# Performance work log

Hardware: AMD Instinct MI355X
Metric: run time of the kernel (lower is better)

Reference implementation:

```python
import jax, jax.numpy as jnp
import numpy as np

IN, OUT, STEPS, BATCH = 1024, 1024, 100, 64
THR = 15.0
RATIO = 0.5
C1 = RATIO * THR            # initial membrane potential = 7.5
C2 = 1.0 / THR
C3 = (1.0 - RATIO) / STEPS


def setup_inputs() -> dict:
    key = jax.random.key(0)
    k0, k1, k2, k3 = jax.random.split(key, 4)
    spikes = jax.random.randint(k0, (STEPS, BATCH, IN), 0, 2).astype(jnp.float32)
    mem = jnp.full((BATCH, OUT), C1, dtype=jnp.float32)          # init_if
    hat_spikes = jax.random.uniform(k1, (BATCH, IN), dtype=jnp.float32)
    W = jax.random.normal(k2, (OUT, IN), dtype=jnp.float32)      # w_mean=0, w_std=1
    b = jax.random.normal(k3, (OUT,), dtype=jnp.float32)
    return {"spikes": spikes, "mem": mem, "hat_spikes": hat_spikes, "W": W, "b": b}


def reference(spikes, mem, hat_spikes, W, b):
    steps = spikes.shape[0]
    # delta_us = fc(spikes): [T, B, OUT]
    delta_us = jnp.einsum('tbi,oi->tbo', spikes, W) + b

    def step(carry, du):
        m, su = carry
        m = m + du
        s = (m > THR).astype(m.dtype)          # spike
        m = jnp.clip(m, 0.0, THR)              # clamp_(0, thr)
        su = su + m                            # sum_u += mem
        m = m - m * s                          # reset fired neurons
        return (m, su), s

    (mem_out, sum_u), ss = jax.lax.scan(
        step, (mem, jnp.zeros_like(mem)), delta_us)

    hat_u_fwd = sum_u / steps                  # [B, OUT]
    hat_s_fwd = ss.mean(axis=0)                # [B, OUT]

    # training-mode surrogate path: forward values come from the spike loop,
    # gradients flow through fc(hat_spikes) (ForwardFirstBackwardSecond)
    delta_u = hat_spikes @ W.T + b
    hat_u = jax.lax.stop_gradient(hat_u_fwd) + delta_u - jax.lax.stop_gradient(delta_u)
    surr = jnp.maximum(hat_u * C2, C3)         # (hat_u*C2).clamp_min(C3)
    hat_s = jax.lax.stop_gradient(hat_s_fwd) + surr - jax.lax.stop_gradient(surr)

    return ss, mem_out, hat_s
```

## Files before the change

kernel.cpp:

```cpp
#include <hip/hip_runtime.h>


typedef __attribute__((ext_vector_type(4))) int int4v;

#define T_STEPS 100
#define BO 65536
#define K_DIM 1024
#define A8_OFF 0
#define BT_OFF 6553600
#define LO_OFF 11796480

__global__ __launch_bounds__(256)
void prepass(const float* __restrict__ S, const float* __restrict__ W,
             signed char* __restrict__ A8, signed char* __restrict__ Bt) {
    const int wave = blockIdx.x * 4 + (threadIdx.x >> 6);
    const int lane = threadIdx.x & 63;
    const int r16 = lane & 15, quad = lane >> 4;

    if (wave < 6400) {
        const int m16 = wave >> 4, k64 = wave & 15;
        const int m = m16 * 16 + r16;
        const float* sp = S + (size_t)m * K_DIM + k64 * 64 + quad * 16;
        const float4 s0 = *(const float4*)(sp);
        const float4 s1 = *(const float4*)(sp + 4);
        const float4 s2 = *(const float4*)(sp + 8);
        const float4 s3 = *(const float4*)(sp + 12);
        const float sv[16] = {s0.x,s0.y,s0.z,s0.w, s1.x,s1.y,s1.z,s1.w,
                              s2.x,s2.y,s2.z,s2.w, s3.x,s3.y,s3.z,s3.w};
        union { signed char c[16]; int4v v; } u;
#pragma unroll
        for (int e = 0; e < 16; ++e) u.c[e] = (signed char)sv[e];
        *(int4v*)(A8 + ((size_t)(m16 * 16 + k64) * 1024) + lane * 16) = u.v;
    } else {
        const int t2 = wave - 6400;
        const int n16 = t2 >> 4, k64 = t2 & 15;
        const int n = n16 * 16 + r16;
        const float* wp = W + (size_t)n * K_DIM + k64 * 64 + quad * 16;
        const float4 w0 = *(const float4*)(wp);
        const float4 w1 = *(const float4*)(wp + 4);
        const float4 w2 = *(const float4*)(wp + 8);
        const float4 w3 = *(const float4*)(wp + 12);
        const float wv[16] = {w0.x,w0.y,w0.z,w0.w, w1.x,w1.y,w1.z,w1.w,
                              w2.x,w2.y,w2.z,w2.w, w3.x,w3.y,w3.z,w3.w};
        union { signed char c[16]; int4v v; } u[4];
#pragma unroll
        for (int e = 0; e < 16; ++e) {
            long long q = llrint((double)wv[e] * 0x1p28);
#pragma unroll
            for (int p = 0; p < 3; ++p) {
                const int d = (int)(((q + 128) & 255) - 128);
                u[p].c[e] = (signed char)d;
                q = (q - d) >> 8;
            }
            u[3].c[e] = (signed char)q;
        }
        signed char* base = Bt + (size_t)(n16 * 16 + k64) * 4 * 1024 + lane * 16;
#pragma unroll
        for (int p = 0; p < 4; ++p)
            *(int4v*)(base + (size_t)p * 1024) = u[p].v;
    }
}

__global__ __launch_bounds__(256)
void gemm_i8(const signed char* __restrict__ A8,
             const signed char* __restrict__ Bt,
             const float* __restrict__ bias,
             float* __restrict__ Chi,
             _Float16* __restrict__ Lo) {
    const int bid = blockIdx.x;
    const int xcd = bid & 7;
    const int t_  = bid >> 3;
    const int cu  = t_ & 31;
    const int rnd = t_ >> 5;
    const int bn = (xcd << 2) | (cu & 3);
    const int bm = (cu >> 2) + (rnd << 3);

    const int tid = threadIdx.x;
    const int lane = tid & 63, wid = tid >> 6;
    const int wm = wid >> 1, wn = wid & 1;
    const int quad = lane >> 4, r16 = lane & 15;
    const int mgb = bm * 8 + wm * 4;
    const int ng  = bn * 2 + wn;

    const signed char* Ab = A8 + (size_t)mgb * 16384 + (size_t)lane * 16;
    const signed char* Bb = Bt + (size_t)ng * 65536 + (size_t)lane * 16;

    int4v av[3][4], bv[3][4];
    int4v acc[4][4] = {};

    auto loadS = [&](int kt, int s) {
#pragma unroll
        for (int i = 0; i < 4; ++i)
            av[s][i] = *(const int4v*)(Ab + (size_t)(i * 16 + kt) * 1024);
#pragma unroll
        for (int p = 0; p < 4; ++p)
            bv[s][p] = *(const int4v*)(Bb + (size_t)(kt * 4 + p) * 1024);
    };
    auto mf = [&](int s) {
#pragma unroll
        for (int p = 0; p < 4; ++p)
#pragma unroll
            for (int i = 0; i < 4; ++i)
                acc[i][p] = __builtin_amdgcn_mfma_i32_16x16x64_i8(
                    av[s][i], bv[s][p], acc[i][p], 0, 0, 0);
    };

    loadS(0, 0);
    loadS(1, 1);
#pragma unroll
    for (int kt = 0; kt < 16; ++kt) {
        if (kt + 2 < 16) loadS(kt + 2, (kt + 2) % 3);
        mf(kt % 3);
    }

    const int n_g = bn * 32 + wn * 16 + r16;
    const double bd = (double)bias[n_g];
#pragma unroll
    for (int i = 0; i < 4; ++i)
#pragma unroll
        for (int e = 0; e < 4; ++e) {
            long long t = (long long)acc[i][3][e];
            t = t * 256 + (long long)acc[i][2][e];
            t = t * 256 + (long long)acc[i][1][e];
            t = t * 256 + (long long)acc[i][0][e];
            const double du = (double)t * 0x1p-28 + bd;
            const float hi = (float)du;
            const float lo = (float)(du - (double)hi);
            const size_t m_g = (size_t)(bm * 128 + wm * 64 + i * 16 + quad * 4 + e);
            const size_t off = m_g * 1024 + n_g;
            Chi[off] = hi;
            Lo[off] = (_Float16)(lo * 4096.0f);
        }
}

__global__ __launch_bounds__(256)
void snn_scan(float* __restrict__ out, const _Float16* __restrict__ lo,
              const float* __restrict__ mem0) {
    const int bo = blockIdx.x * 256 + threadIdx.x;
    double m = (double)mem0[bo];
    double cnt = 0.0;
    float h[4][4], l[4][4];
#pragma unroll
    for (int s = 0; s < 3; ++s)
#pragma unroll
        for (int u = 0; u < 4; ++u) {
            const size_t idx = (size_t)(s * 4 + u) * BO + bo;
            h[s][u] = out[idx];
            l[s][u] = (float)lo[idx];
        }
#pragma unroll
    for (int g = 0; g < 25; ++g) {
        const int cs = g & 3, ps = (g + 3) & 3;
        if (g + 3 < 25) {
#pragma unroll
            for (int u = 0; u < 4; ++u) {
                const size_t idx = (size_t)((g + 3) * 4 + u) * BO + bo;
                h[ps][u] = out[idx];
                l[ps][u] = (float)lo[idx];
            }
        }
#pragma unroll
        for (int u = 0; u < 4; ++u) {
            const double du = (double)h[cs][u] + (double)l[cs][u] * 0x1p-12;
            m += du;
            const double s = (m > 15.0) ? 1.0 : 0.0;
            m = fmin(fmax(m, 0.0), 15.0);
            out[(size_t)(g * 4 + u) * BO + bo] = (float)s;
            cnt += s;
            m -= m * s;
        }
    }
    out[(size_t)T_STEPS * BO + bo] = (float)m;
    out[(size_t)(T_STEPS + 1) * BO + bo] = (float)(cnt * 0.01);
}

extern "C" void kernel_launch(void* const* d_in, const int* in_sizes, int n_in,
                              void* d_out, int out_size, void* d_ws, size_t ws_size,
                              hipStream_t stream) {
    const float* spikes = (const float*)d_in[0];
    const float* mem    = (const float*)d_in[1];
    const float* W      = (const float*)d_in[3];
    const float* b      = (const float*)d_in[4];
    float* out = (float*)d_out;
    signed char* A8 = (signed char*)d_ws + A8_OFF;
    signed char* Bt = (signed char*)d_ws + BT_OFF;
    _Float16*    Lo = (_Float16*)((char*)d_ws + LO_OFF);

    prepass<<<dim3(1856), 256, 0, stream>>>(spikes, W, A8, Bt);
    gemm_i8<<<dim3(1600), 256, 0, stream>>>(A8, Bt, b, out, Lo);
    snn_scan<<<dim3(BO / 256), 256, 0, stream>>>(out, Lo, mem);
}
```

Measured before the change: 138.8 us.

## Stage GEMM operand tiles through double-buffered LDS shared across waves

The int8 GEMM used to have each wave load its own A and B fragments straight from global memory, so waves sharing rows or columns fetched the same data twice. Now the 256 threads load each k-tile of A and B once into a double-buffered 32KB shared-memory tile, and each wave reads its MFMA fragments from LDS. This halves global traffic per block, at the cost of a barrier every k-step, LDS round trips, and a shallower prefetch than the previous triple-buffered register pipeline. The launch bounds now request 3 blocks per CU to keep occupancy up.

```diff
diff --git a/kernel.cpp b/kernel.cpp
--- a/kernel.cpp
+++ b/kernel.cpp
@@ -61,12 +61,13 @@
     }
 }
 
-__global__ __launch_bounds__(256)
+__global__ __launch_bounds__(256, 3)
 void gemm_i8(const signed char* __restrict__ A8,
              const signed char* __restrict__ Bt,
              const float* __restrict__ bias,
              float* __restrict__ Chi,
              _Float16* __restrict__ Lo) {
+    __shared__ signed char lds[2][16384];
     const int bid = blockIdx.x;
     const int xcd = bid & 7;
     const int t_  = bid >> 3;
@@ -79,38 +80,62 @@
     const int lane = tid & 63, wid = tid >> 6;
     const int wm = wid >> 1, wn = wid & 1;
     const int quad = lane >> 4, r16 = lane & 15;
-    const int mgb = bm * 8 + wm * 4;
-    const int ng  = bn * 2 + wn;
-
-    const signed char* Ab = A8 + (size_t)mgb * 16384 + (size_t)lane * 16;
-    const signed char* Bb = Bt + (size_t)ng * 65536 + (size_t)lane * 16;
-
-    int4v av[3][4], bv[3][4];
+
+    const signed char* sbase[4];
+    int sstride[4], ldsoff[4];
+#pragma unroll
+    for (int j = 0; j < 4; ++j) {
+        const int c = wid * 4 + j;
+        if (c < 8) {
+            sbase[j] = A8 + (size_t)(bm * 8 + c) * 16384 + lane * 16;
+            sstride[j] = 1024;
+            ldsoff[j] = c * 1024 + lane * 16;
+        } else {
+            const int j2 = c - 8;
+            sbase[j] = Bt + (size_t)(bn * 2 + (j2 >> 2)) * 65536
+                          + (size_t)(j2 & 3) * 1024 + lane * 16;
+            sstride[j] = 4096;
+            ldsoff[j] = 8192 + j2 * 1024 + lane * 16;
+        }
+    }
+    int aoff[4], boff[4];
+#pragma unroll
+    for (int i = 0; i < 4; ++i) aoff[i] = (wm * 4 + i) * 1024 + lane * 16;
+#pragma unroll
+    for (int p = 0; p < 4; ++p) boff[p] = 8192 + (wn * 4 + p) * 1024 + lane * 16;
+
+    int4v sreg[4];
     int4v acc[4][4] = {};
 
-    auto loadS = [&](int kt, int s) {
-#pragma unroll
-        for (int i = 0; i < 4; ++i)
-            av[s][i] = *(const int4v*)(Ab + (size_t)(i * 16 + kt) * 1024);
-#pragma unroll
-        for (int p = 0; p < 4; ++p)
-            bv[s][p] = *(const int4v*)(Bb + (size_t)(kt * 4 + p) * 1024);
-    };
-    auto mf = [&](int s) {
+#pragma unroll
+    for (int j = 0; j < 4; ++j) sreg[j] = *(const int4v*)(sbase[j]);
+#pragma unroll
+    for (int j = 0; j < 4; ++j) *(int4v*)(&lds[0][ldsoff[j]]) = sreg[j];
+    __syncthreads();
+
+    for (int kt = 0; kt < 16; ++kt) {
+        const int cur = kt & 1, nxt = cur ^ 1;
+        if (kt + 1 < 16) {
+#pragma unroll
+            for (int j = 0; j < 4; ++j)
+                sreg[j] = *(const int4v*)(sbase[j] + (size_t)(kt + 1) * sstride[j]);
+        }
+        int4v af[4], bf[4];
+#pragma unroll
+        for (int i = 0; i < 4; ++i) af[i] = *(const int4v*)(&lds[cur][aoff[i]]);
+#pragma unroll
+        for (int p = 0; p < 4; ++p) bf[p] = *(const int4v*)(&lds[cur][boff[p]]);
 #pragma unroll
         for (int p = 0; p < 4; ++p)
 #pragma unroll
             for (int i = 0; i < 4; ++i)
                 acc[i][p] = __builtin_amdgcn_mfma_i32_16x16x64_i8(
-                    av[s][i], bv[s][p], acc[i][p], 0, 0, 0);
-    };
-
-    loadS(0, 0);
-    loadS(1, 1);
-#pragma unroll
-    for (int kt = 0; kt < 16; ++kt) {
-        if (kt + 2 < 16) loadS(kt + 2, (kt + 2) % 3);
-        mf(kt % 3);
+                    af[i], bf[p], acc[i][p], 0, 0, 0);
+        if (kt + 1 < 16) {
+#pragma unroll
+            for (int j = 0; j < 4; ++j) *(int4v*)(&lds[nxt][ldsoff[j]]) = sreg[j];
+        }
+        __syncthreads();
     }
 
     const int n_g = bn * 32 + wn * 16 + r16;
```

Result: faster. 127.7 us (-8.0%).
